# Performance work log

Measured on AMD Instinct MI355X. Metric: run time of the kernel, lower is better.

Reference implementation:

```python
import jax, jax.numpy as jnp
import numpy as np

B, N, C = 2, 8192, 256
H = 8
CH = C // H  # head dim 32
M = 32       # nbhd size
HID = 512    # mlp hidden = 2.0 * dim
TAB = 3025   # pre_table rows (55x55 relative positions)
POSF = 5     # pos_dim + 3


def _ln(x, w, b):
    mu = jnp.mean(x, axis=-1, keepdims=True)
    var = jnp.var(x, axis=-1, keepdims=True)
    return (x - mu) / jnp.sqrt(var + 1e-5) * w + b


def setup_inputs() -> dict:
    key = jax.random.key(0)
    ks = jax.random.split(key, 24)
    s = lambda fan: 1.0 / np.sqrt(fan)
    inp = {
        'feat': jax.random.normal(ks[0], (B, N, C), jnp.float32),
        'member_idx': jax.random.randint(ks[1], (B, N, M), 0, N),
        'cluster_mask': jnp.ones((B, N, M), jnp.float32),
        'pe_idx': jax.random.randint(ks[2], (B, N, M), 0, TAB),
        'global_attn': 0,
        'pre_table': jax.random.normal(ks[3], (TAB, POSF), jnp.float32),
        'norm1_w': jnp.ones((C,), jnp.float32),
        'norm1_b': jnp.zeros((C,), jnp.float32),
        'q_w': jax.random.normal(ks[4], (C, C), jnp.float32) * s(C),
        'q_b': jnp.zeros((C,), jnp.float32),
        'kv_w': jax.random.normal(ks[5], (2 * C, C), jnp.float32) * s(C),
        'kv_b': jnp.zeros((2 * C,), jnp.float32),
        'blank_k': jax.random.normal(ks[6], (C,), jnp.float32),
        'blank_v': jax.random.normal(ks[7], (C,), jnp.float32),
        'pe_w': jax.random.normal(ks[8], (H, POSF), jnp.float32) * s(POSF),
        'pe_b': jnp.zeros((H,), jnp.float32),
        'proj_w': jax.random.normal(ks[9], (C, C), jnp.float32) * s(C),
        'proj_b': jnp.zeros((C,), jnp.float32),
        'norm2_w': jnp.ones((C,), jnp.float32),
        'norm2_b': jnp.zeros((C,), jnp.float32),
        'fc1_w': jax.random.normal(ks[10], (HID, C), jnp.float32) * s(C),
        'fc1_b': jnp.zeros((HID,), jnp.float32),
        'fc2_w': jax.random.normal(ks[11], (C, HID), jnp.float32) * s(HID),
        'fc2_b': jnp.zeros((C,), jnp.float32),
    }
    return inp


def _block(feat, member_idx, cluster_mask, pe_idx, pre_table,
           norm1_w, norm1_b, q_w, q_b, kv_w, kv_b, blank_k, blank_v,
           pe_w, pe_b, proj_w, proj_b, norm2_w, norm2_b,
           fc1_w, fc1_b, fc2_w, fc2_b):
    b, n, c = feat.shape
    h, c_ = H, c // H
    scale = c_ ** -0.5
    shortcut = feat
    x = _ln(feat, norm1_w, norm1_b)
    q = (x @ q_w.T + q_b) * scale                     # b n c
    kv = (x @ kv_w.T + kv_b).reshape(b, n, h, 2, c_)  # torch view layout
    k = kv[..., 0, :]                                 # b n h c_
    v = kv[..., 1, :]
    q = q.reshape(b, n, h, c_)
    bidx = jnp.arange(b)[:, None, None]
    k_g = k[bidx, member_idx]                         # b n m h c_ (gather)
    attn = jnp.einsum('bnhc,bnmhc->bhnm', q, k_g)     # CLUSTENQK
    pe_table = pre_table @ pe_w.T + pe_b              # TAB h
    pos = pe_table[pe_idx]                            # b n m h
    attn = attn + pos.transpose(0, 3, 1, 2)
    attn = attn + (1.0 - cluster_mask)[:, None, :, :] * (-100.0)
    blank = jnp.einsum('bnhc,hc->bhn', q, blank_k.reshape(h, c_))
    blank = jnp.clip(blank, -5.0, 5.0)[..., None]     # b h n 1
    attn = jnp.concatenate([attn, blank], axis=-1)
    attn = jax.nn.softmax(attn, axis=-1)
    blank_a = attn[..., -1:]
    attn = attn[..., :-1]
    v_g = v[bidx, member_idx]                         # b n m h c_
    out = jnp.einsum('bhnm,bnmhc->bnhc', attn, v_g)   # CLUSTENAV
    out = out + blank_a.transpose(0, 2, 1, 3) * blank_v.reshape(1, 1, h, c_)
    out = out.reshape(b, n, c)
    out = out @ proj_w.T + proj_b
    x = shortcut + out
    y = _ln(x, norm2_w, norm2_b)
    y = jax.nn.gelu(y @ fc1_w.T + fc1_b, approximate=False)
    y = y @ fc2_w.T + fc2_b
    return x + y


def reference(feat, member_idx, cluster_mask, pe_idx, global_attn, pre_table,
              norm1_w, norm1_b, q_w, q_b, kv_w, kv_b, blank_k, blank_v,
              pe_w, pe_b, proj_w, proj_b, norm2_w, norm2_b,
              fc1_w, fc1_b, fc2_w, fc2_b):
    # global_attn is False (local cluster attention path)
    return _block(feat, member_idx, cluster_mask, pe_idx, pre_table,
                  norm1_w, norm1_b, q_w, q_b, kv_w, kv_b, blank_k, blank_v,
                  pe_w, pe_b, proj_w, proj_b, norm2_w, norm2_b,
                  fc1_w, fc1_b, fc2_w, fc2_b)
```

## Files before the change

kernel.cpp:

```cpp
#include <hip/hip_runtime.h>
#include <math.h>

namespace {
constexpr int kN    = 8192;
constexpr int kC    = 256;
constexpr int kRowsTotal = 2 * kN;
constexpr float kScale = 0.17677669529663687f;
}

typedef __attribute__((ext_vector_type(8))) short bf16x8;
typedef __attribute__((ext_vector_type(4))) float f32x4;
typedef _Float16 h8 __attribute__((ext_vector_type(8)));
typedef _Float16 h4 __attribute__((ext_vector_type(4)));
typedef _Float16 h2 __attribute__((ext_vector_type(2)));

__device__ __forceinline__ unsigned short f2bf(float f) {
  unsigned int u = __float_as_uint(f);
  u += 0x7fffu + ((u >> 16) & 1u);
  return (unsigned short)(u >> 16);
}
__device__ __forceinline__ unsigned short f2h(float f) {
  _Float16 h = (_Float16)f;
  unsigned short u;
  __builtin_memcpy(&u, &h, 2);
  return u;
}
__device__ __forceinline__ float h2f(unsigned short u) {
  _Float16 h;
  __builtin_memcpy(&h, &u, 2);
  return (float)h;
}

#if __has_builtin(__builtin_amdgcn_fdot2)
__device__ __forceinline__ float fdot2f(h2 a, h2 b, float c) {
  return __builtin_amdgcn_fdot2(a, b, c, false);
}
#else
__device__ __forceinline__ float fdot2f(h2 a, h2 b, float c) {
  return fmaf((float)a[0], (float)b[0], fmaf((float)a[1], (float)b[1], c));
}
#endif

#define GLOAD16(g, l)                                                   \
  __builtin_amdgcn_global_load_lds(                                     \
      (const __attribute__((address_space(1))) void*)(g),               \
      (__attribute__((address_space(3))) void*)(l), 16, 0, 0)

__global__ __launch_bounds__(256) void prep_kernel(
    const float* __restrict__ qw, const float* __restrict__ kvw,
    const float* __restrict__ pjw, const float* __restrict__ f1w,
    const float* __restrict__ f2w, const float* __restrict__ qb,
    const float* __restrict__ kvb, const float* __restrict__ bk,
    const int* __restrict__ pe_idx, const float* __restrict__ pre_table,
    const float* __restrict__ pe_w, const float* __restrict__ pe_b,
    const float* __restrict__ cmask, unsigned short* __restrict__ wqkv,
    unsigned short* __restrict__ wproj, unsigned short* __restrict__ wfc1,
    unsigned short* __restrict__ wfc2, float* __restrict__ bqkv,
    unsigned short* __restrict__ bkh, unsigned short* __restrict__ posm) {
  int bid = blockIdx.x;
  int t = threadIdx.x;
  if (bid < 2052) {
    int i = bid * 256 + t;
    if (i < 65536)       wqkv[i]            = f2bf(qw[i]);
    else if (i < 196608) wqkv[i]            = f2bf(kvw[i - 65536]);
    else if (i < 262144) wproj[i - 196608]  = f2bf(pjw[i - 196608]);
    else if (i < 393216) wfc1[i - 262144]   = f2bf(f1w[i - 262144]);
    else if (i < 524288) wfc2[i - 393216]   = f2bf(f2w[i - 393216]);
    else if (i < 524544) bqkv[i - 524288]   = qb[i - 524288];
    else if (i < 525056) bqkv[i - 524288]   = kvb[i - 524544];
    else if (i < 525312) bkh[i - 525056]    = f2h(bk[i - 525056]);
  } else {
    int i = (bid - 2052) * 256 + t;
    int row = i >> 8, m = (i >> 3) & 31, h = i & 7;
    int idx = pe_idx[(size_t)row * 32 + m];
    float acc = pe_b[h];
#pragma unroll
    for (int f = 0; f < 5; ++f)
      acc += pre_table[idx * 5 + f] * pe_w[h * 5 + f];
    acc += (1.0f - cmask[(size_t)row * 32 + m]) * -100.0f;
    posm[(size_t)row * 256 + h * 32 + m] = f2h(acc);
  }
}

__global__ __launch_bounds__(512) void qkv_fused(
    const float* __restrict__ feat, const float* __restrict__ n1w,
    const float* __restrict__ n1b, const unsigned short* __restrict__ Wq,
    const float* __restrict__ bqkv, unsigned short* __restrict__ qo,
    unsigned short* __restrict__ ko, unsigned short* __restrict__ vo) {
  __shared__ alignas(16) unsigned short sm[33280];
  int t = threadIdx.x;
  int w = t >> 6, l = t & 63;
  int bm = blockIdx.x * 64;
  const int lr = l & 15, lk = l >> 4;
  const int BsB = 16896;

  {
    int r = t >> 3, sub = t & 7;
    float4 xv[8];
    float sx = 0.f, sxx = 0.f;
#pragma unroll
    for (int i = 0; i < 8; ++i) {
      xv[i] = *(const float4*)(feat + (size_t)(bm + r) * 256 + sub * 4 + i * 32);
      sx  += xv[i].x + xv[i].y + xv[i].z + xv[i].w;
      sxx += xv[i].x * xv[i].x + xv[i].y * xv[i].y + xv[i].z * xv[i].z +
             xv[i].w * xv[i].w;
    }
#pragma unroll
    for (int d = 1; d < 8; d <<= 1) {
      sx  += __shfl_xor(sx, d, 64);
      sxx += __shfl_xor(sxx, d, 64);
    }
    float mu = sx * (1.0f / 256.0f);
    float rstd = rsqrtf(sxx * (1.0f / 256.0f) - mu * mu + 1e-5f);
#pragma unroll
    for (int i = 0; i < 8; ++i) {
      int c = sub * 4 + i * 32;
      float4 wv = *(const float4*)(n1w + c);
      float4 bv = *(const float4*)(n1b + c);
      uint2 ov;
      ov.x = ((unsigned int)f2bf((xv[i].y - mu) * rstd * wv.y + bv.y) << 16) |
             f2bf((xv[i].x - mu) * rstd * wv.x + bv.x);
      ov.y = ((unsigned int)f2bf((xv[i].w - mu) * rstd * wv.w + bv.w) << 16) |
             f2bf((xv[i].z - mu) * rstd * wv.z + bv.z);
      *(uint2*)&sm[r * 264 + c] = ov;
    }
  }

#define QSTAGE(buf, k0, bn)                                                   \
  do {                                                                        \
    GLOAD16(Wq + (size_t)((bn)*256 + w * 32 + (l >> 2)) * 256 + (k0) +        \
                (l & 3) * 8,                                                  \
            sm + BsB + (buf)*8192 + w * 1024 + l * 8);                        \
    GLOAD16(Wq + (size_t)((bn)*256 + w * 32 + 16 + (l >> 2)) * 256 + (k0) +   \
                (l & 3) * 8,                                                  \
            sm + BsB + (buf)*8192 + w * 1024 + 512 + l * 8);                  \
  } while (0)

#pragma unroll
  for (int bn = 0; bn < 3; ++bn) {
    f32x4 acc[4][2] = {};
    auto computeQ = [&](int buf, int ka) {
      bf16x8 af[4], bfr[2];
#pragma unroll
      for (int mi = 0; mi < 4; ++mi)
        af[mi] = *(const bf16x8*)(sm + (mi * 16 + lr) * 264 + ka + lk * 8);
#pragma unroll
      for (int ni = 0; ni < 2; ++ni)
        bfr[ni] = *(const bf16x8*)(sm + BsB + buf * 8192 + w * 1024 +
                                   (ni * 16 + lr) * 32 + lk * 8);
#pragma unroll
      for (int mi = 0; mi < 4; ++mi)
#pragma unroll
        for (int ni = 0; ni < 2; ++ni)
          acc[mi][ni] = __builtin_amdgcn_mfma_f32_16x16x32_bf16(
              af[mi], bfr[ni], acc[mi][ni], 0, 0, 0);
    };
    QSTAGE(0, 0, bn);
    __syncthreads();
    int cur = 0;
#pragma unroll
    for (int k0 = 32; k0 < 256; k0 += 32) {
      QSTAGE(cur ^ 1, k0, bn);
      computeQ(cur, k0 - 32);
      __syncthreads();
      cur ^= 1;
    }
    computeQ(cur, 224);

#pragma unroll
    for (int mi = 0; mi < 4; ++mi) {
#pragma unroll
      for (int ni = 0; ni < 2; ++ni) {
        int col = bn * 256 + w * 32 + ni * 16 + lr;
        float bv = bqkv[col];
#pragma unroll
        for (int j = 0; j < 4; ++j) {
          int rg = bm + mi * 16 + lk * 4 + j;
          float x = acc[mi][ni][j] + bv;
          if (col < 256) {
            qo[(size_t)rg * 256 + col] = f2h(x * kScale);
          } else {
            int c = col - 256;
            int h = c >> 6, sbit = (c >> 5) & 1, ch = c & 31;
            unsigned short* dst = sbit ? vo : ko;
            dst[(size_t)rg * 256 + h * 32 + ch] = f2h(x);
          }
        }
      }
    }
    __syncthreads();
  }
#undef QSTAGE
}

__global__ __launch_bounds__(512) void mlp_fused(
    const unsigned short* __restrict__ A, const unsigned short* __restrict__ Wp,
    const float* __restrict__ pbias, const float* __restrict__ feat,
    const float* __restrict__ w2, const float* __restrict__ b2,
    const unsigned short* __restrict__ W1, const float* __restrict__ b1,
    const unsigned short* __restrict__ W2, const float* __restrict__ b2f,
    float* __restrict__ outp) {
  __shared__ alignas(16) unsigned short sm[66560];
  int t = threadIdx.x;
  int w = t >> 6, l = t & 63;
  int bm = blockIdx.x * 64;
  const int lr = l & 15, lk = l >> 4;

  f32x4 accp[4][2] = {};
  {
    const size_t aoff = (size_t)(bm + w * 8 + (l >> 3)) * 256 + (l & 7) * 8;
    const size_t boff = (size_t)(w * 32 + (l >> 3)) * 256 + (l & 7) * 8;
#define PSTAGE(buf, k0)                                                       \
  do {                                                                        \
    GLOAD16(A + aoff + (k0), sm + (buf)*4096 + w * 512 + l * 8);              \
    GLOAD16(Wp + boff + (k0), sm + 8192 + (buf)*16384 + w * 2048 + l * 8);    \
    GLOAD16(Wp + boff + (k0) + (size_t)2048,                                  \
            sm + 8192 + (buf)*16384 + w * 2048 + 512 + l * 8);                \
    GLOAD16(Wp + boff + (k0) + (size_t)4096,                                  \
            sm + 8192 + (buf)*16384 + w * 2048 + 1024 + l * 8);               \
    GLOAD16(Wp + boff + (k0) + (size_t)6144,                                  \
            sm + 8192 + (buf)*16384 + w * 2048 + 1536 + l * 8);               \
  } while (0)
    auto computeP = [&](int buf) {
#pragma unroll
      for (int kk = 0; kk < 2; ++kk) {
        bf16x8 af[4], bfr[2];
#pragma unroll
        for (int mi = 0; mi < 4; ++mi)
          af[mi] = *(const bf16x8*)(sm + buf * 4096 + (mi * 16 + lr) * 64 +
                                    kk * 32 + lk * 8);
#pragma unroll
        for (int ni = 0; ni < 2; ++ni)
          bfr[ni] = *(const bf16x8*)(sm + 8192 + buf * 16384 +
                                     (w * 32 + ni * 16 + lr) * 64 + kk * 32 +
                                     lk * 8);
#pragma unroll
        for (int mi = 0; mi < 4; ++mi)
#pragma unroll
          for (int ni = 0; ni < 2; ++ni)
            accp[mi][ni] = __builtin_amdgcn_mfma_f32_16x16x32_bf16(
                af[mi], bfr[ni], accp[mi][ni], 0, 0, 0);
      }
    };
    PSTAGE(0, 0);
    __syncthreads();
    int cur = 0;
#pragma unroll
    for (int k0 = 64; k0 < 256; k0 += 64) {
      PSTAGE(cur ^ 1, k0);
      computeP(cur);
      __syncthreads();
      cur ^= 1;
    }
    computeP(cur);
#undef PSTAGE
  }

  f32x4 xr[4][2];
  float* xs = (float*)sm;
  __syncthreads();
#pragma unroll
  for (int mi = 0; mi < 4; ++mi) {
#pragma unroll
    for (int ni = 0; ni < 2; ++ni) {
      int c = w * 32 + ni * 16 + lr;
      float bv = pbias[c];
#pragma unroll
      for (int j = 0; j < 4; ++j) {
        int rl = mi * 16 + lk * 4 + j;
        float x = accp[mi][ni][j] + bv + feat[(size_t)(bm + rl) * 256 + c];
        xr[mi][ni][j] = x;
        xs[rl * 260 + c] = x;
      }
    }
  }
  __syncthreads();

  {
    int r = t >> 3, sub = t & 7;
    float4 xv[8];
    float sx = 0.f, sxx = 0.f;
#pragma unroll
    for (int i = 0; i < 8; ++i) {
      xv[i] = *(const float4*)&xs[r * 260 + sub * 4 + i * 32];
      sx  += xv[i].x + xv[i].y + xv[i].z + xv[i].w;
      sxx += xv[i].x * xv[i].x + xv[i].y * xv[i].y + xv[i].z * xv[i].z +
             xv[i].w * xv[i].w;
    }
#pragma unroll
    for (int d = 1; d < 8; d <<= 1) {
      sx  += __shfl_xor(sx, d, 64);
      sxx += __shfl_xor(sxx, d, 64);
    }
    float mu = sx * (1.0f / 256.0f);
    float rstd = rsqrtf(sxx * (1.0f / 256.0f) - mu * mu + 1e-5f);
#pragma unroll
    for (int i = 0; i < 8; ++i) {
      int c = sub * 4 + i * 32;
      float4 wv = *(const float4*)(w2 + c);
      float4 bv = *(const float4*)(b2 + c);
      uint2 ov;
      ov.x = ((unsigned int)f2bf((xv[i].y - mu) * rstd * wv.y + bv.y) << 16) |
             f2bf((xv[i].x - mu) * rstd * wv.x + bv.x);
      ov.y = ((unsigned int)f2bf((xv[i].w - mu) * rstd * wv.w + bv.w) << 16) |
             f2bf((xv[i].z - mu) * rstd * wv.z + bv.z);
      *(uint2*)&sm[49664 + r * 264 + c] = ov;
    }
  }
  __syncthreads();

  const int FB = 33280;
#define F1STAGE(buf, k0, c)                                                   \
  do {                                                                        \
    GLOAD16(W1 + (size_t)((c)*256 + w * 32 + (l >> 2)) * 256 + (k0) +         \
                (l & 3) * 8,                                                  \
            sm + FB + (buf)*8192 + w * 1024 + l * 8);                         \
    GLOAD16(W1 + (size_t)((c)*256 + w * 32 + 16 + (l >> 2)) * 256 + (k0) +    \
                (l & 3) * 8,                                                  \
            sm + FB + (buf)*8192 + w * 1024 + 512 + l * 8);                   \
  } while (0)
#pragma unroll
  for (int c = 0; c < 2; ++c) {
    f32x4 accf[4][2] = {};
    auto computeF1 = [&](int buf, int ka) {
      bf16x8 af[4], bfr[2];
#pragma unroll
      for (int mi = 0; mi < 4; ++mi)
        af[mi] =
            *(const bf16x8*)(sm + 49664 + (mi * 16 + lr) * 264 + ka + lk * 8);
#pragma unroll
      for (int ni = 0; ni < 2; ++ni)
        bfr[ni] = *(const bf16x8*)(sm + FB + buf * 8192 +
                                   (w * 32 + ni * 16 + lr) * 32 + lk * 8);
#pragma unroll
      for (int mi = 0; mi < 4; ++mi)
#pragma unroll
        for (int ni = 0; ni < 2; ++ni)
          accf[mi][ni] = __builtin_amdgcn_mfma_f32_16x16x32_bf16(
              af[mi], bfr[ni], accf[mi][ni], 0, 0, 0);
    };
    F1STAGE(0, 0, c);
    __syncthreads();
    int cur = 0;
#pragma unroll
    for (int k0 = 32; k0 < 256; k0 += 32) {
      F1STAGE(cur ^ 1, k0, c);
      computeF1(cur, k0 - 32);
      __syncthreads();
      cur ^= 1;
    }
    computeF1(cur, 224);
    __syncthreads();
#pragma unroll
    for (int mi = 0; mi < 4; ++mi) {
#pragma unroll
      for (int ni = 0; ni < 2; ++ni) {
        int colg = c * 256 + w * 32 + ni * 16 + lr;
        float bv = b1[colg];
#pragma unroll
        for (int j = 0; j < 4; ++j) {
          float x = accf[mi][ni][j] + bv;
          float g = 0.5f * x * (1.0f + erff(x * 0.70710678118654752f));
          sm[(mi * 16 + lk * 4 + j) * 520 + colg] = f2bf(g);
        }
      }
    }
  }
#undef F1STAGE
  __syncthreads();

  f32x4 acc2[4][2] = {};
#define F2STAGE(buf, k0)                                                      \
  do {                                                                        \
    GLOAD16(W2 + (size_t)(w * 32 + (l >> 3)) * 512 + (k0) + (l & 7) * 8,      \
            sm + FB + (buf)*16384 + w * 2048 + l * 8);                        \
    GLOAD16(W2 + (size_t)(w * 32 + 8 + (l >> 3)) * 512 + (k0) + (l & 7) * 8,  \
            sm + FB + (buf)*16384 + w * 2048 + 512 + l * 8);                  \
    GLOAD16(W2 + (size_t)(w * 32 + 16 + (l >> 3)) * 512 + (k0) + (l & 7) * 8, \
            sm + FB + (buf)*16384 + w * 2048 + 1024 + l * 8);                 \
    GLOAD16(W2 + (size_t)(w * 32 + 24 + (l >> 3)) * 512 + (k0) + (l & 7) * 8, \
            sm + FB + (buf)*16384 + w * 2048 + 1536 + l * 8);                 \
  } while (0)
  {
    auto computeF2 = [&](int buf, int ka) {
#pragma unroll
      for (int kk = 0; kk < 2; ++kk) {
        bf16x8 af[4], bfr[2];
#pragma unroll
        for (int mi = 0; mi < 4; ++mi)
          af[mi] = *(const bf16x8*)(sm + (mi * 16 + lr) * 520 + ka + kk * 32 +
                                    lk * 8);
#pragma unroll
        for (int ni = 0; ni < 2; ++ni)
          bfr[ni] = *(const bf16x8*)(sm + FB + buf * 16384 +
                                     (w * 32 + ni * 16 + lr) * 64 + kk * 32 +
                                     lk * 8);
#pragma unroll
        for (int mi = 0; mi < 4; ++mi)
#pragma unroll
          for (int ni = 0; ni < 2; ++ni)
            acc2[mi][ni] = __builtin_amdgcn_mfma_f32_16x16x32_bf16(
                af[mi], bfr[ni], acc2[mi][ni], 0, 0, 0);
      }
    };
    F2STAGE(0, 0);
    __syncthreads();
    int cur = 0;
#pragma unroll
    for (int k0 = 64; k0 < 512; k0 += 64) {
      F2STAGE(cur ^ 1, k0);
      computeF2(cur, k0 - 64);
      __syncthreads();
      cur ^= 1;
    }
    computeF2(cur, 448);
  }
#undef F2STAGE

#pragma unroll
  for (int mi = 0; mi < 4; ++mi) {
#pragma unroll
    for (int ni = 0; ni < 2; ++ni) {
      int col = w * 32 + ni * 16 + lr;
      float bv = b2f[col];
#pragma unroll
      for (int j = 0; j < 4; ++j) {
        int rg = bm + mi * 16 + lk * 4 + j;
        outp[(size_t)rg * 256 + col] = xr[mi][ni][j] + acc2[mi][ni][j] + bv;
      }
    }
  }
}

__global__ __launch_bounds__(256) void attn_kernel(
    const unsigned short* __restrict__ q, const unsigned short* __restrict__ k,
    const unsigned short* __restrict__ v, const int* __restrict__ member_idx,
    const unsigned short* __restrict__ posm,
    const unsigned short* __restrict__ bkh, const float* __restrict__ blank_v,
    unsigned short* __restrict__ outp) {
  int t = threadIdx.x;
  int w = t >> 6, l = t & 63;
  int bid = blockIdx.x;
  int part = bid & 7;
  int bb = part >> 2, hg = part & 3;
  int row = bb * kN + (bid >> 3) * 4 + w;
  const unsigned int kvbyte = (unsigned int)bb * (kN * 512u);

  __shared__ float        aw[4][2][36];
  __shared__ unsigned int offs[4][32];
  __shared__ float        posl[4][2][32];

  {
    int m = l & 31, hloc = l >> 5;
    posl[w][hloc][m] = h2f(posm[(size_t)row * 256 + hg * 64 + l]);
    if (l < 32)
      offs[w][l] =
          kvbyte + (unsigned int)member_idx[(size_t)row * 32 + l] * 512u;
  }
  __syncthreads();

  const int m8 = l >> 3, ch = l & 7;
  const int hsel = ch >> 2;

  h8 qv8 = *(const h8*)(q + (size_t)row * 256 + hg * 64 + ch * 8);
  const h2* qa = (const h2*)&qv8;

  float lg[4];
#pragma unroll
  for (int i = 0; i < 4; ++i) {
    int mi = i * 8 + m8;
    const char* kp = (const char*)k + offs[w][mi] + hg * 128 + ch * 16;
    h8 kv = *(const h8*)kp;
    const h2* ka = (const h2*)&kv;
    float p = 0.f;
#pragma unroll
    for (int e = 0; e < 4; ++e) p = fdot2f(qa[e], ka[e], p);
    p += __shfl_xor(p, 1, 64);
    p += __shfl_xor(p, 2, 64);
    lg[i] = p + posl[w][hsel][mi];
  }

  float bl = 0.f;
  {
    h8 bk8 = *(const h8*)(bkh + hg * 64 + ch * 8);
    const h2* ba = (const h2*)&bk8;
#pragma unroll
    for (int e = 0; e < 4; ++e) bl = fdot2f(qa[e], ba[e], bl);
    bl += __shfl_xor(bl, 1, 64);
    bl += __shfl_xor(bl, 2, 64);
    bl = fminf(fmaxf(bl, -5.0f), 5.0f);
  }

  float mx = fmaxf(fmaxf(lg[0], lg[1]), fmaxf(lg[2], lg[3]));
  mx = fmaxf(mx, __shfl_xor(mx, 8, 64));
  mx = fmaxf(mx, __shfl_xor(mx, 16, 64));
  mx = fmaxf(mx, __shfl_xor(mx, 32, 64));
  mx = fmaxf(mx, bl);
  float e4[4], s = 0.f;
#pragma unroll
  for (int i = 0; i < 4; ++i) { e4[i] = __expf(lg[i] - mx); s += e4[i]; }
  s += __shfl_xor(s, 8, 64);
  s += __shfl_xor(s, 16, 64);
  s += __shfl_xor(s, 32, 64);
  float eb = __expf(bl - mx);
  s += eb;
  float inv = __builtin_amdgcn_rcpf(s);
  if ((ch & 3) == 0) {
#pragma unroll
    for (int i = 0; i < 4; ++i) aw[w][hsel][i * 8 + m8] = e4[i] * inv;
    if (m8 == 0) aw[w][hsel][32] = eb * inv;
  }
  __syncthreads();

  const int hp = l >> 5, sq = (l >> 3) & 3, c8 = l & 7;
  const char* vb = (const char*)v + (hg * 2 + hp) * 64 + c8 * 8;
  float a0 = 0.f, a1 = 0.f, a2 = 0.f, a3 = 0.f;
#pragma unroll
  for (int i = 0; i < 8; ++i) {
    int mm = sq * 8 + i;
    float a = aw[w][hp][mm];
    h4 u = *(const h4*)(vb + offs[w][mm]);
    a0 = fmaf(a, (float)u[0], a0);
    a1 = fmaf(a, (float)u[1], a1);
    a2 = fmaf(a, (float)u[2], a2);
    a3 = fmaf(a, (float)u[3], a3);
  }
  a0 += __shfl_xor(a0, 8, 64);  a1 += __shfl_xor(a1, 8, 64);
  a2 += __shfl_xor(a2, 8, 64);  a3 += __shfl_xor(a3, 8, 64);
  a0 += __shfl_xor(a0, 16, 64); a1 += __shfl_xor(a1, 16, 64);
  a2 += __shfl_xor(a2, 16, 64); a3 += __shfl_xor(a3, 16, 64);
  if (sq == 0) {
    float ab = aw[w][hp][32];
    int c = (hg * 2 + hp) * 32 + c8 * 4;
    float4 bv = *(const float4*)(blank_v + c);
    a0 = fmaf(ab, bv.x, a0);
    a1 = fmaf(ab, bv.y, a1);
    a2 = fmaf(ab, bv.z, a2);
    a3 = fmaf(ab, bv.w, a3);
    uint2 o;
    o.x = ((unsigned int)f2bf(a1) << 16) | f2bf(a0);
    o.y = ((unsigned int)f2bf(a3) << 16) | f2bf(a2);
    *(uint2*)(outp + (size_t)row * 256 + c) = o;
  }
}

extern "C" void kernel_launch(void* const* d_in, const int* in_sizes, int n_in,
                              void* d_out, int out_size, void* d_ws, size_t ws_size,
                              hipStream_t stream) {
  const float* feat       = (const float*)d_in[0];
  const int*   member_idx = (const int*)d_in[1];
  const float* cmask      = (const float*)d_in[2];
  const int*   pe_idx     = (const int*)d_in[3];
  const float* pre_table  = (const float*)d_in[5];
  const float* n1w        = (const float*)d_in[6];
  const float* n1b        = (const float*)d_in[7];
  const float* q_w        = (const float*)d_in[8];
  const float* q_b        = (const float*)d_in[9];
  const float* kv_w       = (const float*)d_in[10];
  const float* kv_b       = (const float*)d_in[11];
  const float* blank_k    = (const float*)d_in[12];
  const float* blank_v    = (const float*)d_in[13];
  const float* pe_w       = (const float*)d_in[14];
  const float* pe_b       = (const float*)d_in[15];
  const float* proj_w     = (const float*)d_in[16];
  const float* proj_b     = (const float*)d_in[17];
  const float* n2w        = (const float*)d_in[18];
  const float* n2b        = (const float*)d_in[19];
  const float* fc1_w      = (const float*)d_in[20];
  const float* fc1_b      = (const float*)d_in[21];
  const float* fc2_w      = (const float*)d_in[22];
  const float* fc2_b      = (const float*)d_in[23];

  float* out = (float*)d_out;
  unsigned char* ws = (unsigned char*)d_ws;

  unsigned short* attn_out = (unsigned short*)(ws + 0);
  unsigned short* q_buf = (unsigned short*)(ws + 8388608);
  unsigned short* k_buf = (unsigned short*)(ws + 16777216);
  unsigned short* v_buf = (unsigned short*)(ws + 25165824);
  unsigned short* wqkv  = (unsigned short*)(ws + 33554432);
  unsigned short* wproj = (unsigned short*)(ws + 33947648);
  unsigned short* wfc1  = (unsigned short*)(ws + 34078720);
  unsigned short* wfc2  = (unsigned short*)(ws + 34340864);
  float*          bqkv  = (float*)(ws + 34603008);
  unsigned short* bkh   = (unsigned short*)(ws + 34606080);
  unsigned short* posm  = (unsigned short*)out;

  prep_kernel<<<18436, 256, 0, stream>>>(
      q_w, kv_w, proj_w, fc1_w, fc2_w, q_b, kv_b, blank_k, pe_idx, pre_table,
      pe_w, pe_b, cmask, wqkv, wproj, wfc1, wfc2, bqkv, bkh, posm);

  qkv_fused<<<kRowsTotal / 64, 512, 0, stream>>>(
      feat, n1w, n1b, wqkv, bqkv, q_buf, k_buf, v_buf);

  attn_kernel<<<kRowsTotal, 256, 0, stream>>>(
      q_buf, k_buf, v_buf, member_idx, posm, bkh, blank_v, attn_out);

  mlp_fused<<<kRowsTotal / 64, 512, 0, stream>>>(
      attn_out, wproj, proj_b, feat, n2w, n2b, wfc1, fc1_b, wfc2, fc2_b, out);
}
```

Before: 110.7 us.

## Halve GEMM row tiles and split MLP into proj+LN2 and FC kernels

Row tiles in the QKV and MLP GEMM kernels shrink from 64 to 32 rows, doubling the grid to 512 blocks and cutting shared memory and accumulator registers so more blocks fit per CU. The activation tiles move into a k-chunked [k/32][row][32] shared layout. The single fused MLP kernel is split in two. The first does the projection, residual and LayerNorm2, writing x and a bf16 LN output to global memory. The second runs fc1, GELU and fc2 and accumulates into the output. This trades extra global traffic, an extra launch and twice as many weight reloads per row for higher occupancy and parallelism.

New measurement: 121.6 us. 1.1x slower.

```diff
diff --git a/kernel.cpp b/kernel.cpp
--- a/kernel.cpp
+++ b/kernel.cpp
@@ -87,34 +87,33 @@
     const float* __restrict__ n1b, const unsigned short* __restrict__ Wq,
     const float* __restrict__ bqkv, unsigned short* __restrict__ qo,
     unsigned short* __restrict__ ko, unsigned short* __restrict__ vo) {
-  __shared__ alignas(16) unsigned short sm[33280];
+  __shared__ alignas(16) unsigned short sm[24576];
   int t = threadIdx.x;
   int w = t >> 6, l = t & 63;
-  int bm = blockIdx.x * 64;
+  int bm = blockIdx.x * 32;
   const int lr = l & 15, lk = l >> 4;
-  const int BsB = 16896;
 
   {
-    int r = t >> 3, sub = t & 7;
-    float4 xv[8];
+    int r = t >> 4, sub = t & 15;
+    float4 xv[4];
     float sx = 0.f, sxx = 0.f;
 #pragma unroll
-    for (int i = 0; i < 8; ++i) {
-      xv[i] = *(const float4*)(feat + (size_t)(bm + r) * 256 + sub * 4 + i * 32);
+    for (int i = 0; i < 4; ++i) {
+      xv[i] = *(const float4*)(feat + (size_t)(bm + r) * 256 + sub * 4 + i * 64);
       sx  += xv[i].x + xv[i].y + xv[i].z + xv[i].w;
       sxx += xv[i].x * xv[i].x + xv[i].y * xv[i].y + xv[i].z * xv[i].z +
              xv[i].w * xv[i].w;
     }
 #pragma unroll
-    for (int d = 1; d < 8; d <<= 1) {
+    for (int d = 1; d < 16; d <<= 1) {
       sx  += __shfl_xor(sx, d, 64);
       sxx += __shfl_xor(sxx, d, 64);
     }
     float mu = sx * (1.0f / 256.0f);
     float rstd = rsqrtf(sxx * (1.0f / 256.0f) - mu * mu + 1e-5f);
 #pragma unroll
-    for (int i = 0; i < 8; ++i) {
-      int c = sub * 4 + i * 32;
+    for (int i = 0; i < 4; ++i) {
+      int c = sub * 4 + i * 64;
       float4 wv = *(const float4*)(n1w + c);
       float4 bv = *(const float4*)(n1b + c);
       uint2 ov;
@@ -122,7 +121,7 @@
              f2bf((xv[i].x - mu) * rstd * wv.x + bv.x);
       ov.y = ((unsigned int)f2bf((xv[i].w - mu) * rstd * wv.w + bv.w) << 16) |
              f2bf((xv[i].z - mu) * rstd * wv.z + bv.z);
-      *(uint2*)&sm[r * 264 + c] = ov;
+      *(uint2*)&sm[(c >> 5) * 1024 + r * 32 + (c & 31)] = ov;
     }
   }
 
@@ -130,26 +129,27 @@
   do {                                                                        \
     GLOAD16(Wq + (size_t)((bn)*256 + w * 32 + (l >> 2)) * 256 + (k0) +        \
                 (l & 3) * 8,                                                  \
-            sm + BsB + (buf)*8192 + w * 1024 + l * 8);                        \
+            sm + 8192 + (buf)*8192 + w * 1024 + l * 8);                       \
     GLOAD16(Wq + (size_t)((bn)*256 + w * 32 + 16 + (l >> 2)) * 256 + (k0) +   \
                 (l & 3) * 8,                                                  \
-            sm + BsB + (buf)*8192 + w * 1024 + 512 + l * 8);                  \
+            sm + 8192 + (buf)*8192 + w * 1024 + 512 + l * 8);                 \
   } while (0)
 
 #pragma unroll
   for (int bn = 0; bn < 3; ++bn) {
-    f32x4 acc[4][2] = {};
+    f32x4 acc[2][2] = {};
     auto computeQ = [&](int buf, int ka) {
-      bf16x8 af[4], bfr[2];
-#pragma unroll
-      for (int mi = 0; mi < 4; ++mi)
-        af[mi] = *(const bf16x8*)(sm + (mi * 16 + lr) * 264 + ka + lk * 8);
+      bf16x8 af[2], bfr[2];
+#pragma unroll
+      for (int mi = 0; mi < 2; ++mi)
+        af[mi] = *(const bf16x8*)(sm + (ka >> 5) * 1024 + (mi * 16 + lr) * 32 +
+                                  lk * 8);
 #pragma unroll
       for (int ni = 0; ni < 2; ++ni)
-        bfr[ni] = *(const bf16x8*)(sm + BsB + buf * 8192 + w * 1024 +
-                                   (ni * 16 + lr) * 32 + lk * 8);
-#pragma unroll
-      for (int mi = 0; mi < 4; ++mi)
+        bfr[ni] = *(const bf16x8*)(sm + 8192 + buf * 8192 +
+                                   (w * 32 + ni * 16 + lr) * 32 + lk * 8);
+#pragma unroll
+      for (int mi = 0; mi < 2; ++mi)
 #pragma unroll
         for (int ni = 0; ni < 2; ++ni)
           acc[mi][ni] = __builtin_amdgcn_mfma_f32_16x16x32_bf16(
@@ -168,7 +168,7 @@
     computeQ(cur, 224);
 
 #pragma unroll
-    for (int mi = 0; mi < 4; ++mi) {
+    for (int mi = 0; mi < 2; ++mi) {
 #pragma unroll
       for (int ni = 0; ni < 2; ++ni) {
         int col = bn * 256 + w * 32 + ni * 16 + lr;
@@ -193,74 +193,68 @@
 #undef QSTAGE
 }
 
-__global__ __launch_bounds__(512) void mlp_fused(
+__global__ __launch_bounds__(512) void proj_ln2(
     const unsigned short* __restrict__ A, const unsigned short* __restrict__ Wp,
     const float* __restrict__ pbias, const float* __restrict__ feat,
     const float* __restrict__ w2, const float* __restrict__ b2,
-    const unsigned short* __restrict__ W1, const float* __restrict__ b1,
-    const unsigned short* __restrict__ W2, const float* __restrict__ b2f,
-    float* __restrict__ outp) {
-  __shared__ alignas(16) unsigned short sm[66560];
+    float* __restrict__ x_out, unsigned short* __restrict__ yln) {
+  __shared__ alignas(16) unsigned short sm[24576];
   int t = threadIdx.x;
   int w = t >> 6, l = t & 63;
-  int bm = blockIdx.x * 64;
+  int bm = blockIdx.x * 32;
   const int lr = l & 15, lk = l >> 4;
 
-  f32x4 accp[4][2] = {};
-  {
-    const size_t aoff = (size_t)(bm + w * 8 + (l >> 3)) * 256 + (l & 7) * 8;
-    const size_t boff = (size_t)(w * 32 + (l >> 3)) * 256 + (l & 7) * 8;
+#pragma unroll
+  for (int g = 0; g < 2; ++g) {
+    int chunk = g * 4 + (t >> 7);
+    int row = (t >> 2) & 31;
+    GLOAD16(A + (size_t)(bm + row) * 256 + chunk * 32 + (t & 3) * 8,
+            sm + g * 4096 + w * 512 + l * 8);
+  }
+
 #define PSTAGE(buf, k0)                                                       \
   do {                                                                        \
-    GLOAD16(A + aoff + (k0), sm + (buf)*4096 + w * 512 + l * 8);              \
-    GLOAD16(Wp + boff + (k0), sm + 8192 + (buf)*16384 + w * 2048 + l * 8);    \
-    GLOAD16(Wp + boff + (k0) + (size_t)2048,                                  \
-            sm + 8192 + (buf)*16384 + w * 2048 + 512 + l * 8);                \
-    GLOAD16(Wp + boff + (k0) + (size_t)4096,                                  \
-            sm + 8192 + (buf)*16384 + w * 2048 + 1024 + l * 8);               \
-    GLOAD16(Wp + boff + (k0) + (size_t)6144,                                  \
-            sm + 8192 + (buf)*16384 + w * 2048 + 1536 + l * 8);               \
+    GLOAD16(Wp + (size_t)(w * 32 + (l >> 2)) * 256 + (k0) + (l & 3) * 8,      \
+            sm + 8192 + (buf)*8192 + w * 1024 + l * 8);                       \
+    GLOAD16(Wp + (size_t)(w * 32 + 16 + (l >> 2)) * 256 + (k0) + (l & 3) * 8, \
+            sm + 8192 + (buf)*8192 + w * 1024 + 512 + l * 8);                 \
   } while (0)
-    auto computeP = [&](int buf) {
-#pragma unroll
-      for (int kk = 0; kk < 2; ++kk) {
-        bf16x8 af[4], bfr[2];
-#pragma unroll
-        for (int mi = 0; mi < 4; ++mi)
-          af[mi] = *(const bf16x8*)(sm + buf * 4096 + (mi * 16 + lr) * 64 +
-                                    kk * 32 + lk * 8);
-#pragma unroll
-        for (int ni = 0; ni < 2; ++ni)
-          bfr[ni] = *(const bf16x8*)(sm + 8192 + buf * 16384 +
-                                     (w * 32 + ni * 16 + lr) * 64 + kk * 32 +
-                                     lk * 8);
-#pragma unroll
-        for (int mi = 0; mi < 4; ++mi)
-#pragma unroll
-          for (int ni = 0; ni < 2; ++ni)
-            accp[mi][ni] = __builtin_amdgcn_mfma_f32_16x16x32_bf16(
-                af[mi], bfr[ni], accp[mi][ni], 0, 0, 0);
-      }
-    };
-    PSTAGE(0, 0);
+
+  f32x4 acc[2][2] = {};
+  auto computeP = [&](int buf, int ka) {
+    bf16x8 af[2], bfr[2];
+#pragma unroll
+    for (int mi = 0; mi < 2; ++mi)
+      af[mi] = *(const bf16x8*)(sm + (ka >> 5) * 1024 + (mi * 16 + lr) * 32 +
+                                lk * 8);
+#pragma unroll
+    for (int ni = 0; ni < 2; ++ni)
+      bfr[ni] = *(const bf16x8*)(sm + 8192 + buf * 8192 +
+                                 (w * 32 + ni * 16 + lr) * 32 + lk * 8);
+#pragma unroll
+    for (int mi = 0; mi < 2; ++mi)
+#pragma unroll
+      for (int ni = 0; ni < 2; ++ni)
+        acc[mi][ni] = __builtin_amdgcn_mfma_f32_16x16x32_bf16(
+            af[mi], bfr[ni], acc[mi][ni], 0, 0, 0);
+  };
+  PSTAGE(0, 0);
+  __syncthreads();
+  int cur = 0;
+#pragma unroll
+  for (int k0 = 32; k0 < 256; k0 += 32) {
+    PSTAGE(cur ^ 1, k0);
+    computeP(cur, k0 - 32);
     __syncthreads();
-    int cur = 0;
-#pragma unroll
-    for (int k0 = 64; k0 < 256; k0 += 64) {
-      PSTAGE(cur ^ 1, k0);
-      computeP(cur);
-      __syncthreads();
-      cur ^= 1;
-    }
-    computeP(cur);
+    cur ^= 1;
+  }
+  computeP(cur, 224);
 #undef PSTAGE
-  }
-
-  f32x4 xr[4][2];
+
+  __syncthreads();
   float* xs = (float*)sm;
-  __syncthreads();
-#pragma unroll
-  for (int mi = 0; mi < 4; ++mi) {
+#pragma unroll
+  for (int mi = 0; mi < 2; ++mi) {
 #pragma unroll
     for (int ni = 0; ni < 2; ++ni) {
       int c = w * 32 + ni * 16 + lr;
@@ -268,35 +262,35 @@
 #pragma unroll
       for (int j = 0; j < 4; ++j) {
         int rl = mi * 16 + lk * 4 + j;
-        float x = accp[mi][ni][j] + bv + feat[(size_t)(bm + rl) * 256 + c];
-        xr[mi][ni][j] = x;
+        float x = acc[mi][ni][j] + bv + feat[(size_t)(bm + rl) * 256 + c];
         xs[rl * 260 + c] = x;
+        x_out[(size_t)(bm + rl) * 256 + c] = x;
       }
     }
   }
   __syncthreads();
 
   {
-    int r = t >> 3, sub = t & 7;
-    float4 xv[8];
+    int r = t >> 4, sub = t & 15;
+    float4 xv[4];
     float sx = 0.f, sxx = 0.f;
 #pragma unroll
-    for (int i = 0; i < 8; ++i) {
-      xv[i] = *(const float4*)&xs[r * 260 + sub * 4 + i * 32];
+    for (int i = 0; i < 4; ++i) {
+      xv[i] = *(const float4*)&xs[r * 260 + sub * 4 + i * 64];
       sx  += xv[i].x + xv[i].y + xv[i].z + xv[i].w;
       sxx += xv[i].x * xv[i].x + xv[i].y * xv[i].y + xv[i].z * xv[i].z +
              xv[i].w * xv[i].w;
     }
 #pragma unroll
-    for (int d = 1; d < 8; d <<= 1) {
+    for (int d = 1; d < 16; d <<= 1) {
       sx  += __shfl_xor(sx, d, 64);
       sxx += __shfl_xor(sxx, d, 64);
     }
     float mu = sx * (1.0f / 256.0f);
     float rstd = rsqrtf(sxx * (1.0f / 256.0f) - mu * mu + 1e-5f);
 #pragma unroll
-    for (int i = 0; i < 8; ++i) {
-      int c = sub * 4 + i * 32;
+    for (int i = 0; i < 4; ++i) {
+      int c = sub * 4 + i * 64;
       float4 wv = *(const float4*)(w2 + c);
       float4 bv = *(const float4*)(b2 + c);
       uint2 ov;
@@ -304,121 +298,122 @@
              f2bf((xv[i].x - mu) * rstd * wv.x + bv.x);
       ov.y = ((unsigned int)f2bf((xv[i].w - mu) * rstd * wv.w + bv.w) << 16) |
              f2bf((xv[i].z - mu) * rstd * wv.z + bv.z);
-      *(uint2*)&sm[49664 + r * 264 + c] = ov;
-    }
-  }
-  __syncthreads();
-
-  const int FB = 33280;
-#define F1STAGE(buf, k0, c)                                                   \
+      *(uint2*)(yln + (size_t)(bm + r) * 256 + c) = ov;
+    }
+  }
+}
+
+__global__ __launch_bounds__(512) void fc_fused(
+    const unsigned short* __restrict__ yln, const unsigned short* __restrict__ W1,
+    const float* __restrict__ b1, const unsigned short* __restrict__ W2,
+    const float* __restrict__ b2f, float* __restrict__ xio) {
+  __shared__ alignas(16) unsigned short sm[40960];
+  int t = threadIdx.x;
+  int w = t >> 6, l = t & 63;
+  int bm = blockIdx.x * 32;
+  const int lr = l & 15, lk = l >> 4;
+
+#pragma unroll
+  for (int g = 0; g < 2; ++g) {
+    int chunk = g * 4 + (t >> 7);
+    int row = (t >> 2) & 31;
+    GLOAD16(yln + (size_t)(bm + row) * 256 + chunk * 32 + (t & 3) * 8,
+            sm + 32768 + g * 4096 + w * 512 + l * 8);
+  }
+
+#define WSTAGE(buf, src, ldw, rowoff, k0)                                     \
   do {                                                                        \
-    GLOAD16(W1 + (size_t)((c)*256 + w * 32 + (l >> 2)) * 256 + (k0) +         \
+    GLOAD16((src) + (size_t)((rowoff) + w * 32 + (l >> 2)) * (ldw) + (k0) +   \
                 (l & 3) * 8,                                                  \
-            sm + FB + (buf)*8192 + w * 1024 + l * 8);                         \
-    GLOAD16(W1 + (size_t)((c)*256 + w * 32 + 16 + (l >> 2)) * 256 + (k0) +    \
-                (l & 3) * 8,                                                  \
-            sm + FB + (buf)*8192 + w * 1024 + 512 + l * 8);                   \
+            sm + 16384 + (buf)*8192 + w * 1024 + l * 8);                      \
+    GLOAD16((src) + (size_t)((rowoff) + w * 32 + 16 + (l >> 2)) * (ldw) +     \
+                (k0) + (l & 3) * 8,                                           \
+            sm + 16384 + (buf)*8192 + w * 1024 + 512 + l * 8);                \
   } while (0)
+
 #pragma unroll
   for (int c = 0; c < 2; ++c) {
-    f32x4 accf[4][2] = {};
+    f32x4 accf[2][2] = {};
     auto computeF1 = [&](int buf, int ka) {
-      bf16x8 af[4], bfr[2];
-#pragma unroll
-      for (int mi = 0; mi < 4; ++mi)
-        af[mi] =
-            *(const bf16x8*)(sm + 49664 + (mi * 16 + lr) * 264 + ka + lk * 8);
+      bf16x8 af[2], bfr[2];
+#pragma unroll
+      for (int mi = 0; mi < 2; ++mi)
+        af[mi] = *(const bf16x8*)(sm + 32768 + (ka >> 5) * 1024 +
+                                  (mi * 16 + lr) * 32 + lk * 8);
 #pragma unroll
       for (int ni = 0; ni < 2; ++ni)
-        bfr[ni] = *(const bf16x8*)(sm + FB + buf * 8192 +
+        bfr[ni] = *(const bf16x8*)(sm + 16384 + buf * 8192 +
                                    (w * 32 + ni * 16 + lr) * 32 + lk * 8);
 #pragma unroll
-      for (int mi = 0; mi < 4; ++mi)
+      for (int mi = 0; mi < 2; ++mi)
 #pragma unroll
         for (int ni = 0; ni < 2; ++ni)
           accf[mi][ni] = __builtin_amdgcn_mfma_f32_16x16x32_bf16(
               af[mi], bfr[ni], accf[mi][ni], 0, 0, 0);
     };
-    F1STAGE(0, 0, c);
+    WSTAGE(0, W1, 256, c * 256, 0);
     __syncthreads();
     int cur = 0;
 #pragma unroll
     for (int k0 = 32; k0 < 256; k0 += 32) {
-      F1STAGE(cur ^ 1, k0, c);
+      WSTAGE(cur ^ 1, W1, 256, c * 256, k0);
       computeF1(cur, k0 - 32);
       __syncthreads();
       cur ^= 1;
     }
     computeF1(cur, 224);
-    __syncthreads();
-#pragma unroll
-    for (int mi = 0; mi < 4; ++mi) {
+#pragma unroll
+    for (int mi = 0; mi < 2; ++mi) {
 #pragma unroll
       for (int ni = 0; ni < 2; ++ni) {
-        int colg = c * 256 + w * 32 + ni * 16 + lr;
-        float bv = b1[colg];
+        int cl = w * 32 + ni * 16 + lr;
+        float bv = b1[c * 256 + cl];
 #pragma unroll
         for (int j = 0; j < 4; ++j) {
+          int row = mi * 16 + lk * 4 + j;
           float x = accf[mi][ni][j] + bv;
           float g = 0.5f * x * (1.0f + erff(x * 0.70710678118654752f));
-          sm[(mi * 16 + lk * 4 + j) * 520 + colg] = f2bf(g);
+          int colg = c * 256 + cl;
+          sm[(colg >> 5) * 1024 + row * 32 + (colg & 31)] = f2bf(g);
         }
       }
     }
-  }
-#undef F1STAGE
+    __syncthreads();
+  }
+
+  f32x4 acc2[2][2] = {};
+  auto computeF2 = [&](int buf, int ka) {
+    bf16x8 af[2], bfr[2];
+#pragma unroll
+    for (int mi = 0; mi < 2; ++mi)
+      af[mi] = *(const bf16x8*)(sm + (ka >> 5) * 1024 + (mi * 16 + lr) * 32 +
+                                lk * 8);
+#pragma unroll
+    for (int ni = 0; ni < 2; ++ni)
+      bfr[ni] = *(const bf16x8*)(sm + 16384 + buf * 8192 +
+                                 (w * 32 + ni * 16 + lr) * 32 + lk * 8);
+#pragma unroll
+    for (int mi = 0; mi < 2; ++mi)
+#pragma unroll
+      for (int ni = 0; ni < 2; ++ni)
+        acc2[mi][ni] = __builtin_amdgcn_mfma_f32_16x16x32_bf16(
+            af[mi], bfr[ni], acc2[mi][ni], 0, 0, 0);
+  };
+  WSTAGE(0, W2, 512, 0, 0);
   __syncthreads();
-
-  f32x4 acc2[4][2] = {};
-#define F2STAGE(buf, k0)                                                      \
-  do {                                                                        \
-    GLOAD16(W2 + (size_t)(w * 32 + (l >> 3)) * 512 + (k0) + (l & 7) * 8,      \
-            sm + FB + (buf)*16384 + w * 2048 + l * 8);                        \
-    GLOAD16(W2 + (size_t)(w * 32 + 8 + (l >> 3)) * 512 + (k0) + (l & 7) * 8,  \
-            sm + FB + (buf)*16384 + w * 2048 + 512 + l * 8);                  \
-    GLOAD16(W2 + (size_t)(w * 32 + 16 + (l >> 3)) * 512 + (k0) + (l & 7) * 8, \
-            sm + FB + (buf)*16384 + w * 2048 + 1024 + l * 8);                 \
-    GLOAD16(W2 + (size_t)(w * 32 + 24 + (l >> 3)) * 512 + (k0) + (l & 7) * 8, \
-            sm + FB + (buf)*16384 + w * 2048 + 1536 + l * 8);                 \
-  } while (0)
-  {
-    auto computeF2 = [&](int buf, int ka) {
-#pragma unroll
-      for (int kk = 0; kk < 2; ++kk) {
-        bf16x8 af[4], bfr[2];
-#pragma unroll
-        for (int mi = 0; mi < 4; ++mi)
-          af[mi] = *(const bf16x8*)(sm + (mi * 16 + lr) * 520 + ka + kk * 32 +
-                                    lk * 8);
-#pragma unroll
-        for (int ni = 0; ni < 2; ++ni)
-          bfr[ni] = *(const bf16x8*)(sm + FB + buf * 16384 +
-                                     (w * 32 + ni * 16 + lr) * 64 + kk * 32 +
-                                     lk * 8);
-#pragma unroll
-        for (int mi = 0; mi < 4; ++mi)
-#pragma unroll
-          for (int ni = 0; ni < 2; ++ni)
-            acc2[mi][ni] = __builtin_amdgcn_mfma_f32_16x16x32_bf16(
-                af[mi], bfr[ni], acc2[mi][ni], 0, 0, 0);
-      }
-    };
-    F2STAGE(0, 0);
+  int cur = 0;
+#pragma unroll
+  for (int k0 = 32; k0 < 512; k0 += 32) {
+    WSTAGE(cur ^ 1, W2, 512, 0, k0);
+    computeF2(cur, k0 - 32);
     __syncthreads();
-    int cur = 0;
-#pragma unroll
-    for (int k0 = 64; k0 < 512; k0 += 64) {
-      F2STAGE(cur ^ 1, k0);
-      computeF2(cur, k0 - 64);
-      __syncthreads();
-      cur ^= 1;
-    }
-    computeF2(cur, 448);
-  }
-#undef F2STAGE
-
-#pragma unroll
-  for (int mi = 0; mi < 4; ++mi) {
+    cur ^= 1;
+  }
+  computeF2(cur, 480);
+#undef WSTAGE
+
+#pragma unroll
+  for (int mi = 0; mi < 2; ++mi) {
 #pragma unroll
     for (int ni = 0; ni < 2; ++ni) {
       int col = w * 32 + ni * 16 + lr;
@@ -426,7 +421,8 @@
 #pragma unroll
       for (int j = 0; j < 4; ++j) {
         int rg = bm + mi * 16 + lk * 4 + j;
-        outp[(size_t)rg * 256 + col] = xr[mi][ni][j] + acc2[mi][ni][j] + bv;
+        xio[(size_t)rg * 256 + col] =
+            xio[(size_t)rg * 256 + col] + acc2[mi][ni][j] + bv;
       }
     }
   }
@@ -585,17 +581,21 @@
   float*          bqkv  = (float*)(ws + 34603008);
   unsigned short* bkh   = (unsigned short*)(ws + 34606080);
   unsigned short* posm  = (unsigned short*)out;
+  unsigned short* yln   = q_buf;
 
   prep_kernel<<<18436, 256, 0, stream>>>(
       q_w, kv_w, proj_w, fc1_w, fc2_w, q_b, kv_b, blank_k, pe_idx, pre_table,
       pe_w, pe_b, cmask, wqkv, wproj, wfc1, wfc2, bqkv, bkh, posm);
 
-  qkv_fused<<<kRowsTotal / 64, 512, 0, stream>>>(
+  qkv_fused<<<kRowsTotal / 32, 512, 0, stream>>>(
       feat, n1w, n1b, wqkv, bqkv, q_buf, k_buf, v_buf);
 
   attn_kernel<<<kRowsTotal, 256, 0, stream>>>(
       q_buf, k_buf, v_buf, member_idx, posm, bkh, blank_v, attn_out);
 
-  mlp_fused<<<kRowsTotal / 64, 512, 0, stream>>>(
-      attn_out, wproj, proj_b, feat, n2w, n2b, wfc1, fc1_b, wfc2, fc2_b, out);
-}
+  proj_ln2<<<kRowsTotal / 32, 512, 0, stream>>>(
+      attn_out, wproj, proj_b, feat, n2w, n2b, out, yln);
+
+  fc_fused<<<kRowsTotal / 32, 512, 0, stream>>>(
+      yln, wfc1, fc1_b, wfc2, fc2_b, out);
+}
```
